# Performance work log

Hardware: AMD Instinct MI355X
Metric: run time of the kernel (lower is better)

## Reference

```python
import jax, jax.numpy as jnp
import numpy as np

B, S, D, H = 2, 2048, 768, 12
DH = D // H


def setup_inputs() -> dict:
    key = jax.random.key(0)
    ks = jax.random.split(key, 12)
    f32 = jnp.float32
    sd = 1.0 / np.sqrt(D)
    return {
        "q": jax.random.normal(ks[0], (B, S, D), f32),
        "k": jax.random.normal(ks[1], (B, S, D), f32),
        "v": jax.random.normal(ks[2], (B, S, D), f32),
        "mask": jax.random.normal(ks[3], (S, S), f32),
        "Wq": jax.random.normal(ks[4], (D, D), f32) * sd,
        "bq": jnp.zeros((D,), f32),
        "Wk": jax.random.normal(ks[5], (D, D), f32) * sd,
        "bk": jnp.zeros((D,), f32),
        "Wv": jax.random.normal(ks[6], (D, D), f32) * sd,
        "bv": jnp.zeros((D,), f32),
        "Wo": jax.random.normal(ks[7], (D, D), f32) * sd,
        "bo": jnp.zeros((D,), f32),
    }


def reference(q, k, v, mask, Wq, bq, Wk, bk, Wv, bv, Wo, bo):
    # torch nn.Linear: y = x @ W.T + b
    qh = (q @ Wq.T + bq).reshape(B, S, H, DH).transpose(0, 2, 1, 3)  # [B,H,S,DH]
    kh = (k @ Wk.T + bk).reshape(B, S, H, DH).transpose(0, 2, 1, 3)
    vh = (v @ Wv.T + bv).reshape(B, S, H, DH).transpose(0, 2, 1, 3)
    scores = jnp.einsum("bhsd,bhtd->bhst", qh, kh)  # [B,H,S,S]
    # original adds mask after permute to [H,B,S,S]; with an [S,S] mask the
    # broadcast add is identical either way
    scores = scores + mask
    attn = jax.nn.softmax(scores.astype(jnp.float32) / np.sqrt(DH), axis=-1)
    out = jnp.einsum("bhst,bhtd->bhsd", attn, vh)  # [B,H,S,DH]
    out = out.transpose(0, 2, 1, 3).reshape(B, S, D)
    return out @ Wo.T + bo
```

## Files before the change

kernel.cpp:

```cpp
#include <hip/hip_runtime.h>
#include <hip/hip_bf16.h>

#define B_ 2
#define S_ 2048
#define D_ 768
#define H_ 12
#define DH_ 64
#define M_ (B_*S_)
#define BH_ (B_*H_)

typedef __bf16 v8bf __attribute__((ext_vector_type(8)));
typedef __bf16 v4bf __attribute__((ext_vector_type(4)));
typedef float  v4f  __attribute__((ext_vector_type(4)));
typedef float  f32x16 __attribute__((ext_vector_type(16)));

static __device__ __forceinline__ v4f mfma16(v8bf a, v8bf b, v4f c) {
  return __builtin_amdgcn_mfma_f32_16x16x32_bf16(a, b, c, 0, 0, 0);
}
static __device__ __forceinline__ f32x16 mfma32(v8bf a, v8bf b, f32x16 c) {
  return __builtin_amdgcn_mfma_f32_32x32x16_bf16(a, b, c, 0, 0, 0);
}

static __device__ __forceinline__ void gload_lds16(const __bf16* g, __bf16* l) {
  __builtin_amdgcn_global_load_lds(
      (const __attribute__((address_space(1))) unsigned int*)g,
      (__attribute__((address_space(3))) unsigned int*)l,
      16, 0, 0);
}

#define C1_ 0.18033688011112042f

__global__ __launch_bounds__(256) void convert_kernel(
    const float* __restrict__ q, const float* __restrict__ k, const float* __restrict__ v,
    const float* __restrict__ Wq, const float* __restrict__ Wk,
    const float* __restrict__ Wv, const float* __restrict__ Wo,
    __bf16* __restrict__ Xq, __bf16* __restrict__ Xk, __bf16* __restrict__ Xv,
    __bf16* __restrict__ Wqb, __bf16* __restrict__ Wkb,
    __bf16* __restrict__ Wvb, __bf16* __restrict__ Wob)
{
  const float* src; __bf16* dst; int n;
  switch (blockIdx.y) {
    case 0: src = q;  dst = Xq;  n = M_*D_; break;
    case 1: src = k;  dst = Xk;  n = M_*D_; break;
    case 2: src = v;  dst = Xv;  n = M_*D_; break;
    case 3: src = Wq; dst = Wqb; n = D_*D_; break;
    case 4: src = Wk; dst = Wkb; n = D_*D_; break;
    case 5: src = Wv; dst = Wvb; n = D_*D_; break;
    default: src = Wo; dst = Wob; n = D_*D_; break;
  }
  int n4 = n >> 2;
  for (int i = blockIdx.x*blockDim.x + threadIdx.x; i < n4; i += gridDim.x*blockDim.x) {
    float4 x = ((const float4*)src)[i];
    v4bf y;
    y[0] = (__bf16)x.x; y[1] = (__bf16)x.y; y[2] = (__bf16)x.z; y[3] = (__bf16)x.w;
    ((v4bf*)dst)[i] = y;
  }
}

__global__ __launch_bounds__(256) void em_kernel(
    const float* __restrict__ mask, __bf16* __restrict__ em)
{
  int t = blockIdx.x*256 + threadIdx.x;
  int L = t & 63; int rest = t >> 6;
  int w = rest & 3; rest >>= 2;
  int kt = rest & 63; rest >>= 6;
  int qt = rest;
  int row = qt*128 + w*32 + (L & 31);
  int key0 = kt*32 + ((L >> 5) << 2);
  const float* mp = mask + (size_t)row*S_ + key0;
  float4 m0 = *(const float4*)(mp);
  float4 m1 = *(const float4*)(mp + 8);
  float4 m2 = *(const float4*)(mp + 16);
  float4 m3 = *(const float4*)(mp + 24);
  v8bf e0, e1;
  e0[0] = (__bf16)exp2f(C1_*m0.x); e0[1] = (__bf16)exp2f(C1_*m0.y);
  e0[2] = (__bf16)exp2f(C1_*m0.z); e0[3] = (__bf16)exp2f(C1_*m0.w);
  e0[4] = (__bf16)exp2f(C1_*m1.x); e0[5] = (__bf16)exp2f(C1_*m1.y);
  e0[6] = (__bf16)exp2f(C1_*m1.z); e0[7] = (__bf16)exp2f(C1_*m1.w);
  e1[0] = (__bf16)exp2f(C1_*m2.x); e1[1] = (__bf16)exp2f(C1_*m2.y);
  e1[2] = (__bf16)exp2f(C1_*m2.z); e1[3] = (__bf16)exp2f(C1_*m2.w);
  e1[4] = (__bf16)exp2f(C1_*m3.x); e1[5] = (__bf16)exp2f(C1_*m3.y);
  e1[6] = (__bf16)exp2f(C1_*m3.z); e1[7] = (__bf16)exp2f(C1_*m3.w);
  *(v8bf*)(em + (size_t)t*16)     = e0;
  *(v8bf*)(em + (size_t)t*16 + 8) = e1;
}

static __device__ __forceinline__ void gemm128_pipe(
    const __bf16* __restrict__ A, const __bf16* __restrict__ W,
    int m0, int n0, __bf16* lds, v4f acc[4][4])
{
  const int lane = threadIdx.x & 63;
  const int wave = threadIdx.x >> 6;
  const int r16 = lane & 15;
  const int kc8 = (lane >> 4) << 3;
  const int ia = (wave >> 1) << 2;
  const int ib = (wave & 1) << 2;

  const __bf16* gsrc[4]; int ldo[4];
  #pragma unroll
  for (int t = 0; t < 4; t++) {
    int fb = wave*4 + t;
    gsrc[t] = (fb < 8)
        ? A + (size_t)(m0 + fb*16 + r16)*D_ + kc8
        : W + (size_t)(n0 + (fb - 8)*16 + r16)*D_ + kc8;
    ldo[t] = fb << 9;
  }

  asm volatile("" ::: "memory");
  #pragma unroll
  for (int t = 0; t < 4; t++) gload_lds16(gsrc[t], lds + ldo[t]);
  asm volatile("" ::: "memory");
  #pragma unroll
  for (int t = 0; t < 4; t++) gload_lds16(gsrc[t] + 32, lds + 8192 + ldo[t]);
  asm volatile("" ::: "memory");

#define G_STEP(CUR, NXTB, KC, ISSUE, WSTR) { \
    asm volatile("s_waitcnt vmcnt(" WSTR ")" ::: "memory"); \
    __builtin_amdgcn_s_barrier(); \
    asm volatile("" ::: "memory"); \
    if (ISSUE) { \
      _Pragma("unroll") \
      for (int t = 0; t < 4; t++) \
        gload_lds16(gsrc[t] + (KC), lds + (NXTB)*8192 + ldo[t]); \
    } \
    const __bf16* buf = lds + (CUR)*8192; \
    v8bf a[4], b[4]; \
    _Pragma("unroll") \
    for (int i = 0; i < 4; i++) a[i] = *(const v8bf*)(buf + ((ia+i) << 9) + lane*8); \
    _Pragma("unroll") \
    for (int j = 0; j < 4; j++) b[j] = *(const v8bf*)(buf + ((8+ib+j) << 9) + lane*8); \
    _Pragma("unroll") \
    for (int i = 0; i < 4; i++) \
      _Pragma("unroll") \
      for (int j = 0; j < 4; j++) \
        acc[i][j] = mfma16(a[i], b[j], acc[i][j]); \
  }

  #pragma unroll 1
  for (int ks0 = 0; ks0 < 18; ks0 += 3) {
    G_STEP(0, 2, (ks0+2)*32, true, "4");
    G_STEP(1, 0, (ks0+3)*32, true, "4");
    G_STEP(2, 1, (ks0+4)*32, true, "4");
  }
  G_STEP(0, 2, 20*32, true,  "4");
  G_STEP(1, 0, 21*32, true,  "4");
  G_STEP(2, 1, 22*32, true,  "4");
  G_STEP(0, 2, 23*32, true,  "4");
  G_STEP(1, 0, 0,     false, "4");
  G_STEP(2, 0, 0,     false, "0");
#undef G_STEP
}

__global__ __launch_bounds__(256, 3) void qkv_gemm(
    const __bf16* __restrict__ Xq, const __bf16* __restrict__ Xk, const __bf16* __restrict__ Xv,
    const __bf16* __restrict__ Wqb, const __bf16* __restrict__ Wkb, const __bf16* __restrict__ Wvb,
    const float* __restrict__ bq, const float* __restrict__ bk, const float* __restrict__ bv,
    __bf16* __restrict__ qf, __bf16* __restrict__ kf, __bf16* __restrict__ vf)
{
  __shared__ __bf16 lds[3*8192];
  const int mode = blockIdx.z;
  const __bf16* A = (mode == 0) ? Xq : (mode == 1) ? Xk : Xv;
  const __bf16* W = (mode == 0) ? Wqb : (mode == 1) ? Wkb : Wvb;
  const float* bias = (mode == 0) ? bq : (mode == 1) ? bk : bv;
  const int m0 = blockIdx.y << 7, n0 = blockIdx.x << 7;
  v4f acc[4][4];
  #pragma unroll
  for (int i = 0; i < 4; i++)
    #pragma unroll
    for (int j = 0; j < 4; j++) { v4f z = {0.f,0.f,0.f,0.f}; acc[i][j] = z; }
  gemm128_pipe(A, W, m0, n0, lds, acc);

  const int lane = threadIdx.x & 63;
  const int wave = threadIdx.x >> 6;
  const int wm = (wave >> 1) << 6, wn = (wave & 1) << 6;
  const int col = lane & 15, quad = lane >> 4;
  float bb[4]; int nn[4];
  #pragma unroll
  for (int j = 0; j < 4; j++) { nn[j] = n0 + wn + 16*j + col; bb[j] = bias[nn[j]]; }

  if (mode < 2) {
    __bf16* dst = (mode == 0) ? qf : kf;
    const float sc = (mode == 0) ? C1_ : 1.0f;
    #pragma unroll
    for (int i = 0; i < 4; i++)
      #pragma unroll
      for (int r = 0; r < 4; r++) {
        int m = m0 + wm + 16*i + quad*4 + r;
        int batch = m >> 11, s = m & (S_-1);
        int q32 = s >> 5, s31 = s & 31;
        #pragma unroll
        for (int j = 0; j < 4; j++) {
          int n = nn[j];
          int h = n >> 6, dd = n & 63;
          size_t flat = (((size_t)(batch*H_ + h)*64 + q32)*4 + (dd >> 4))*512
                      + ((((dd >> 3) & 1)*32 + s31) << 3) + (dd & 7);
          dst[flat] = (__bf16)((acc[i][j][r] + bb[j]) * sc);
        }
      }
  } else {
    #pragma unroll
    for (int i = 0; i < 4; i++) {
      int mbase = m0 + wm + 16*i + quad*4;
      int batch = mbase >> 11, s0 = mbase & (S_-1);
      #pragma unroll
      for (int j = 0; j < 4; j++) {
        int n = nn[j];
        int h = n >> 6, dd = n & 63;
        v4bf pk;
        #pragma unroll
        for (int r = 0; r < 4; r++) pk[r] = (__bf16)(acc[i][j][r] + bb[j]);
        size_t flat = ((((size_t)(batch*H_ + h)*64 + (s0 >> 5))*2 + (dd >> 5))*2 + ((s0 >> 4) & 1))*512
                    + ((((s0 >> 3) & 1)*32 + (dd & 31)) << 3) + (s0 & 7);
        *(v4bf*)(vf + flat) = pk;
      }
    }
  }
}

__global__ __launch_bounds__(256, 2) void attn_kernel(
    const __bf16* __restrict__ qf, const __bf16* __restrict__ kf, const __bf16* __restrict__ vf,
    const __bf16* __restrict__ em, __bf16* __restrict__ ao)
{
  __shared__ __bf16 kv[4][2][2048];

  const int bh = blockIdx.y;
  const int qt = blockIdx.x;
  const int wave = threadIdx.x >> 6, lane = threadIdx.x & 63;
  const int q5 = lane & 31, hi = lane >> 5;
  const int batch = bh / H_, h = bh % H_;
  const __bf16* qfb = qf + (size_t)bh * (S_*DH_);
  const __bf16* kfb = kf + (size_t)bh * (S_*DH_);
  const __bf16* vfb = vf + (size_t)bh * (S_*DH_);
  const __bf16* emw = em + (size_t)qt*262144 + wave*1024 + lane*16;

  const int q32 = qt*4 + wave;
  v8bf Qb[4];
  #pragma unroll
  for (int s4 = 0; s4 < 4; s4++)
    Qb[s4] = *(const v8bf*)(qfb + ((size_t)q32*4 + s4)*512 + lane*8);

  const __bf16* gK = kfb + wave*512 + lane*8;
  const __bf16* gV = vfb + wave*512 + lane*8;
  __bf16* kd[4]; __bf16* vd[4];
  #pragma unroll
  for (int b = 0; b < 4; b++) { kd[b] = &kv[b][0][wave*512]; vd[b] = &kv[b][1][wave*512]; }

  f32x16 O0, O1;
  #pragma unroll
  for (int z = 0; z < 16; z++) { O0[z] = 0.f; O1[z] = 0.f; }
  float li = 0.f;

  asm volatile("" ::: "memory");
  gload_lds16(gK, kd[0]);
  gload_lds16(gV, vd[0]);
  v8bf e0a = *(const v8bf*)(emw);
  v8bf e0b = *(const v8bf*)(emw + 8);
  asm volatile("" ::: "memory");
  gload_lds16(gK + 2048, kd[1]);
  gload_lds16(gV + 2048, vd[1]);
  v8bf e1a = *(const v8bf*)(emw + 4096);
  v8bf e1b = *(const v8bf*)(emw + 4104);
  v8bf e2a, e2b, e3a, e3b;

#define ATT_STEP(P, EA, EB, NA, NB, ISSUE, WSTR) \
  { \
    asm volatile("s_waitcnt vmcnt(" WSTR ")" ::: "memory"); \
    __builtin_amdgcn_s_barrier(); \
    asm volatile("" ::: "memory"); \
    if (ISSUE) { \
      const int nkt = kt0 + (P) + 2; \
      gload_lds16(gK + (size_t)nkt*2048, kd[((P)+2)&3]); \
      gload_lds16(gV + (size_t)nkt*2048, vd[((P)+2)&3]); \
      NA = *(const v8bf*)(emw + (size_t)nkt*4096); \
      NB = *(const v8bf*)(emw + (size_t)nkt*4096 + 8); \
    } \
    const __bf16* Kb = kv[(P)&3][0]; \
    const __bf16* Vb = kv[(P)&3][1]; \
    f32x16 Sx; \
    _Pragma("unroll") \
    for (int z = 0; z < 16; z++) Sx[z] = 0.f; \
    _Pragma("unroll") \
    for (int s4 = 0; s4 < 4; s4++) { \
      v8bf Ka = *(const v8bf*)(Kb + s4*512 + lane*8); \
      Sx = mfma32(Ka, Qb[s4], Sx); \
    } \
    float p[16]; float rs = 0.f; \
    _Pragma("unroll") \
    for (int r = 0; r < 8; r++) p[r] = exp2f(Sx[r]) * (float)EA[r]; \
    _Pragma("unroll") \
    for (int r = 0; r < 8; r++) p[8+r] = exp2f(Sx[8+r]) * (float)EB[r]; \
    _Pragma("unroll") \
    for (int r = 0; r < 16; r++) rs += p[r]; \
    li += rs; \
    unsigned g0,g1,g2,g3,g4,g5,g6,g7; \
    { union { __bf16 hh[2]; unsigned u; } t_; \
      t_.hh[0]=(__bf16)p[0];  t_.hh[1]=(__bf16)p[1];  g0=t_.u; \
      t_.hh[0]=(__bf16)p[2];  t_.hh[1]=(__bf16)p[3];  g1=t_.u; \
      t_.hh[0]=(__bf16)p[4];  t_.hh[1]=(__bf16)p[5];  g2=t_.u; \
      t_.hh[0]=(__bf16)p[6];  t_.hh[1]=(__bf16)p[7];  g3=t_.u; \
      t_.hh[0]=(__bf16)p[8];  t_.hh[1]=(__bf16)p[9];  g4=t_.u; \
      t_.hh[0]=(__bf16)p[10]; t_.hh[1]=(__bf16)p[11]; g5=t_.u; \
      t_.hh[0]=(__bf16)p[12]; t_.hh[1]=(__bf16)p[13]; g6=t_.u; \
      t_.hh[0]=(__bf16)p[14]; t_.hh[1]=(__bf16)p[15]; g7=t_.u; } \
    unsigned x0 = __shfl_xor(g0, 32), x1 = __shfl_xor(g1, 32); \
    unsigned x2 = __shfl_xor(g2, 32), x3 = __shfl_xor(g3, 32); \
    unsigned x4 = __shfl_xor(g4, 32), x5 = __shfl_xor(g5, 32); \
    unsigned x6 = __shfl_xor(g6, 32), x7 = __shfl_xor(g7, 32); \
    union { unsigned u[4]; v8bf v; } bp0, bp1; \
    bp0.u[0] = hi ? x2 : g0;    \
    bp0.u[1] = hi ? x3 : g1;    \
    bp0.u[2] = hi ? g2 : x0;    \
    bp0.u[3] = hi ? g3 : x1;    \
    bp1.u[0] = hi ? x6 : g4; \
    bp1.u[1] = hi ? x7 : g5; \
    bp1.u[2] = hi ? g6 : x4; \
    bp1.u[3] = hi ? g7 : x5; \
    v8bf Va00 = *(const v8bf*)(Vb + lane*8); \
    v8bf Va01 = *(const v8bf*)(Vb + 512 + lane*8); \
    v8bf Va10 = *(const v8bf*)(Vb + 1024 + lane*8); \
    v8bf Va11 = *(const v8bf*)(Vb + 1536 + lane*8); \
    O0 = mfma32(Va00, bp0.v, O0); \
    O0 = mfma32(Va01, bp1.v, O0); \
    O1 = mfma32(Va10, bp0.v, O1); \
    O1 = mfma32(Va11, bp1.v, O1); \
  }

  #pragma unroll 1
  for (int kt0 = 0; kt0 < 60; kt0 += 4) {
    ATT_STEP(0, e0a, e0b, e2a, e2b, true, "4");
    ATT_STEP(1, e1a, e1b, e3a, e3b, true, "4");
    ATT_STEP(2, e2a, e2b, e0a, e0b, true, "4");
    ATT_STEP(3, e3a, e3b, e1a, e1b, true, "4");
  }
  {
    const int kt0 = 60;
    ATT_STEP(0, e0a, e0b, e2a, e2b, true,  "4");
    ATT_STEP(1, e1a, e1b, e3a, e3b, true,  "4");
    ATT_STEP(2, e2a, e2b, e0a, e0b, false, "4");
    ATT_STEP(3, e3a, e3b, e1a, e1b, false, "0");
  }
#undef ATT_STEP

  li += __shfl_xor(li, 32);
  float invl = 1.f / li;
  const int qg = qt*128 + wave*32 + q5;
  __bf16* orow = ao + ((size_t)batch*S_ + qg)*D_ + h*DH_;
  #pragma unroll
  for (int g = 0; g < 4; g++) {
    v4bf o0, o1;
    #pragma unroll
    for (int r = 0; r < 4; r++) {
      o0[r] = (__bf16)(O0[g*4+r] * invl);
      o1[r] = (__bf16)(O1[g*4+r] * invl);
    }
    *(v4bf*)(orow + g*8 + hi*4)      = o0;
    *(v4bf*)(orow + 32 + g*8 + hi*4) = o1;
  }
}

__global__ __launch_bounds__(256, 3) void out_gemm(
    const __bf16* __restrict__ Ao, const __bf16* __restrict__ Wob,
    const float* __restrict__ bo, float* __restrict__ out)
{
  __shared__ __bf16 lds[3*8192];
  const int m0 = blockIdx.y << 7, n0 = blockIdx.x << 7;
  v4f acc[4][4];
  #pragma unroll
  for (int i = 0; i < 4; i++)
    #pragma unroll
    for (int j = 0; j < 4; j++) { v4f z = {0.f,0.f,0.f,0.f}; acc[i][j] = z; }
  gemm128_pipe(Ao, Wob, m0, n0, lds, acc);

  const int lane = threadIdx.x & 63;
  const int wave = threadIdx.x >> 6;
  const int wm = (wave >> 1) << 6, wn = (wave & 1) << 6;
  const int col = lane & 15, quad = lane >> 4;
  float bb[4]; int nn[4];
  #pragma unroll
  for (int j = 0; j < 4; j++) { nn[j] = n0 + wn + 16*j + col; bb[j] = bo[nn[j]]; }
  #pragma unroll
  for (int i = 0; i < 4; i++)
    #pragma unroll
    for (int r = 0; r < 4; r++) {
      int m = m0 + wm + 16*i + quad*4 + r;
      #pragma unroll
      for (int j = 0; j < 4; j++)
        out[(size_t)m*D_ + nn[j]] = acc[i][j][r] + bb[j];
    }
}

extern "C" void kernel_launch(void* const* d_in, const int* in_sizes, int n_in,
                              void* d_out, int out_size, void* d_ws, size_t ws_size,
                              hipStream_t stream)
{
  const float* q    = (const float*)d_in[0];
  const float* k    = (const float*)d_in[1];
  const float* v    = (const float*)d_in[2];
  const float* mask = (const float*)d_in[3];
  const float* Wq   = (const float*)d_in[4];
  const float* bq   = (const float*)d_in[5];
  const float* Wk   = (const float*)d_in[6];
  const float* bk   = (const float*)d_in[7];
  const float* Wv   = (const float*)d_in[8];
  const float* bv   = (const float*)d_in[9];
  const float* Wo   = (const float*)d_in[10];
  const float* bo   = (const float*)d_in[11];

  const size_t XN = (size_t)M_ * D_;
  const size_t WN = (size_t)D_ * D_;
  const size_t HN = (size_t)BH_ * S_ * DH_;

  char* ws = (char*)d_ws;
  __bf16* Xq  = (__bf16*)ws;                 ws += XN * 2;
  __bf16* Xk  = (__bf16*)ws;                 ws += XN * 2;
  __bf16* Xv  = (__bf16*)ws;                 ws += XN * 2;
  __bf16* Wqb = (__bf16*)ws;                 ws += WN * 2;
  __bf16* Wkb = (__bf16*)ws;                 ws += WN * 2;
  __bf16* Wvb = (__bf16*)ws;                 ws += WN * 2;
  __bf16* Wob = (__bf16*)ws;                 ws += WN * 2;
  __bf16* qfb = (__bf16*)ws;                 ws += HN * 2;
  __bf16* kfb = (__bf16*)ws;                 ws += HN * 2;
  __bf16* vfb = (__bf16*)ws;                 ws += HN * 2;
  __bf16* aob = (__bf16*)ws;                 ws += XN * 2;
  __bf16* emb = Xq;

  convert_kernel<<<dim3(768, 7), 256, 0, stream>>>(
      q, k, v, Wq, Wk, Wv, Wo, Xq, Xk, Xv, Wqb, Wkb, Wvb, Wob);
  qkv_gemm<<<dim3(6, 32, 3), 256, 0, stream>>>(
      Xq, Xk, Xv, Wqb, Wkb, Wvb, bq, bk, bv, qfb, kfb, vfb);
  em_kernel<<<dim3(1024), 256, 0, stream>>>(mask, emb);
  attn_kernel<<<dim3(16, 24), 256, 0, stream>>>(qfb, kfb, vfb, emb, aob);
  out_gemm<<<dim3(6, 32), 256, 0, stream>>>(aob, Wob, bo, (float*)d_out);
}
```

Measured before the change: 248.1 us.

## Split attention key range across two wave groups and merge partials through LDS

The attention block grows from 4 to 8 waves. The two halves of the block each process half of the key/value tiles (32 of 64) for the same 128 queries, using separate LDS buffers and mask slices. At the end, the upper half writes its partial O accumulators and row sums to LDS, and the lower half adds them, normalises and stores. This halves the serial loop length per block and raises the number of waves in flight. The costs are an LDS reduction step, doubled LDS buffers, and a tighter register budget from launch_bounds(512,4), which could cause spills.

```diff
diff --git a/kernel.cpp b/kernel.cpp
--- a/kernel.cpp
+++ b/kernel.cpp
@@ -217,33 +217,38 @@
   }
 }
 
-__global__ __launch_bounds__(256, 2) void attn_kernel(
+__global__ __launch_bounds__(512, 4) void attn_kernel(
     const __bf16* __restrict__ qf, const __bf16* __restrict__ kf, const __bf16* __restrict__ vf,
     const __bf16* __restrict__ em, __bf16* __restrict__ ao)
 {
-  __shared__ __bf16 kv[4][2][2048];
+  __shared__ __bf16 kv[4][2][2][2048];
 
   const int bh = blockIdx.y;
   const int qt = blockIdx.x;
   const int wave = threadIdx.x >> 6, lane = threadIdx.x & 63;
+  const int qg = wave & 3, half = wave >> 2;
   const int q5 = lane & 31, hi = lane >> 5;
   const int batch = bh / H_, h = bh % H_;
   const __bf16* qfb = qf + (size_t)bh * (S_*DH_);
   const __bf16* kfb = kf + (size_t)bh * (S_*DH_);
   const __bf16* vfb = vf + (size_t)bh * (S_*DH_);
-  const __bf16* emw = em + (size_t)qt*262144 + wave*1024 + lane*16;
-
-  const int q32 = qt*4 + wave;
+  const __bf16* emw = em + (size_t)qt*262144 + (size_t)half*131072
+                         + qg*1024 + lane*16;
+
+  const int q32 = qt*4 + qg;
   v8bf Qb[4];
   #pragma unroll
   for (int s4 = 0; s4 < 4; s4++)
     Qb[s4] = *(const v8bf*)(qfb + ((size_t)q32*4 + s4)*512 + lane*8);
 
-  const __bf16* gK = kfb + wave*512 + lane*8;
-  const __bf16* gV = vfb + wave*512 + lane*8;
+  const __bf16* gK = kfb + (size_t)(half*32)*2048 + qg*512 + lane*8;
+  const __bf16* gV = vfb + (size_t)(half*32)*2048 + qg*512 + lane*8;
   __bf16* kd[4]; __bf16* vd[4];
   #pragma unroll
-  for (int b = 0; b < 4; b++) { kd[b] = &kv[b][0][wave*512]; vd[b] = &kv[b][1][wave*512]; }
+  for (int b = 0; b < 4; b++) {
+    kd[b] = &kv[b][half][0][qg*512];
+    vd[b] = &kv[b][half][1][qg*512];
+  }
 
   f32x16 O0, O1;
   #pragma unroll
@@ -274,8 +279,8 @@
       NA = *(const v8bf*)(emw + (size_t)nkt*4096); \
       NB = *(const v8bf*)(emw + (size_t)nkt*4096 + 8); \
     } \
-    const __bf16* Kb = kv[(P)&3][0]; \
-    const __bf16* Vb = kv[(P)&3][1]; \
+    const __bf16* Kb = &kv[(P)&3][half][0][0]; \
+    const __bf16* Vb = &kv[(P)&3][half][1][0]; \
     f32x16 Sx; \
     _Pragma("unroll") \
     for (int z = 0; z < 16; z++) Sx[z] = 0.f; \
@@ -326,14 +331,14 @@
   }
 
   #pragma unroll 1
-  for (int kt0 = 0; kt0 < 60; kt0 += 4) {
+  for (int kt0 = 0; kt0 < 28; kt0 += 4) {
     ATT_STEP(0, e0a, e0b, e2a, e2b, true, "4");
     ATT_STEP(1, e1a, e1b, e3a, e3b, true, "4");
     ATT_STEP(2, e2a, e2b, e0a, e0b, true, "4");
     ATT_STEP(3, e3a, e3b, e1a, e1b, true, "4");
   }
   {
-    const int kt0 = 60;
+    const int kt0 = 28;
     ATT_STEP(0, e0a, e0b, e2a, e2b, true,  "4");
     ATT_STEP(1, e1a, e1b, e3a, e3b, true,  "4");
     ATT_STEP(2, e2a, e2b, e0a, e0b, false, "4");
@@ -342,19 +347,40 @@
 #undef ATT_STEP
 
   li += __shfl_xor(li, 32);
-  float invl = 1.f / li;
-  const int qg = qt*128 + wave*32 + q5;
-  __bf16* orow = ao + ((size_t)batch*S_ + qg)*D_ + h*DH_;
-  #pragma unroll
-  for (int g = 0; g < 4; g++) {
-    v4bf o0, o1;
-    #pragma unroll
-    for (int r = 0; r < 4; r++) {
-      o0[r] = (__bf16)(O0[g*4+r] * invl);
-      o1[r] = (__bf16)(O1[g*4+r] * invl);
+  __syncthreads();
+  float* cf = (float*)kv;
+  if (half) {
+    float* po = cf + qg*2048;
+    #pragma unroll
+    for (int z = 0; z < 16; z++) {
+      po[z*64 + lane]        = O0[z];
+      po[(16+z)*64 + lane]   = O1[z];
     }
-    *(v4bf*)(orow + g*8 + hi*4)      = o0;
-    *(v4bf*)(orow + 32 + g*8 + hi*4) = o1;
+    cf[8192 + qg*64 + lane] = li;
+  }
+  __syncthreads();
+  if (!half) {
+    const float* po = cf + qg*2048;
+    #pragma unroll
+    for (int z = 0; z < 16; z++) {
+      O0[z] += po[z*64 + lane];
+      O1[z] += po[(16+z)*64 + lane];
+    }
+    li += cf[8192 + qg*64 + lane];
+    float invl = 1.f / li;
+    const int qgl = qt*128 + qg*32 + q5;
+    __bf16* orow = ao + ((size_t)batch*S_ + qgl)*D_ + h*DH_;
+    #pragma unroll
+    for (int g = 0; g < 4; g++) {
+      v4bf o0, o1;
+      #pragma unroll
+      for (int r = 0; r < 4; r++) {
+        o0[r] = (__bf16)(O0[g*4+r] * invl);
+        o1[r] = (__bf16)(O1[g*4+r] * invl);
+      }
+      *(v4bf*)(orow + g*8 + hi*4)      = o0;
+      *(v4bf*)(orow + 32 + g*8 + hi*4) = o1;
+    }
   }
 }
 
@@ -429,6 +455,6 @@
   qkv_gemm<<<dim3(6, 32, 3), 256, 0, stream>>>(
       Xq, Xk, Xv, Wqb, Wkb, Wvb, bq, bk, bv, qfb, kfb, vfb);
   em_kernel<<<dim3(1024), 256, 0, stream>>>(mask, emb);
-  attn_kernel<<<dim3(16, 24), 256, 0, stream>>>(qfb, kfb, vfb, emb, aob);
+  attn_kernel<<<dim3(16, 24), 512, 0, stream>>>(qfb, kfb, vfb, emb, aob);
   out_gemm<<<dim3(6, 32), 256, 0, stream>>>(aob, Wob, bo, (float*)d_out);
 }
```

Measured after the change: 397.0 us. 1.6x slower.
